# Optimization experiments

Hardware: AMD Instinct MI355X
Metric: run time of the kernel (lower is better)

## Reference

```python
import jax, jax.numpy as jnp
import numpy as np

N_HEADS = 8
D_MODEL = 128
EPS = 1e-6


def setup_inputs() -> dict:
    key = jax.random.key(0)
    k1, k2, k3, k4, k5 = jax.random.split(key, 5)
    B, Dim, F, T = 1, D_MODEL, 256, 1024
    queries = jax.random.normal(k1, (B, Dim, F, T), dtype=jnp.float32)
    keys = jax.random.normal(k2, (B, Dim, F, T), dtype=jnp.float32)
    values = jax.random.normal(k3, (B, Dim, F, T), dtype=jnp.float32)
    # out_projection: Linear(d_model, d_output) with d_output == d_model
    W_out = jax.random.normal(k4, (D_MODEL, D_MODEL), dtype=jnp.float32) / np.sqrt(D_MODEL)
    b_out = jax.random.normal(k5, (D_MODEL,), dtype=jnp.float32) * 0.01
    return {"queries": queries, "keys": keys, "values": values,
            "W_out": W_out, "b_out": b_out}


def _to_heads(x, B, Dim, L, H):
    # (B, Dim, F, T) -> (B, L, Dim) -> (B, L, H, d) -> (B, H, L, d)
    return x.reshape(B, Dim, L).transpose(0, 2, 1).reshape(B, L, H, Dim // H).transpose(0, 2, 1, 3)


def reference(queries, keys, values, W_out, b_out):
    B, Dim, F, T = queries.shape
    L = F * T
    H = N_HEADS
    q = jax.nn.sigmoid(_to_heads(queries, B, Dim, L, H))  # (B,H,L,d)
    k = jax.nn.sigmoid(_to_heads(keys, B, Dim, L, H))
    v = _to_heads(values, B, Dim, L, H)

    # NOTE: sums are over the HEAD axis (dim=1), faithful to the original code
    ks = k.sum(axis=1, keepdims=True)                      # (B,1,L,d)
    qs = q.sum(axis=1, keepdims=True)
    sink_incoming = 1.0 / jnp.sum((q + EPS) * (ks + EPS), axis=-1)      # (B,H,L)
    source_outgoing = 1.0 / jnp.sum((k + EPS) * (qs + EPS), axis=-1)    # (B,H,L)
    conserved_sink = jnp.sum(
        (q + EPS) * ((k * source_outgoing[..., None]).sum(axis=1, keepdims=True) + EPS),
        axis=-1)                                                        # (B,H,L)
    conserved_source = jnp.sum(
        (k + EPS) * ((q * sink_incoming[..., None]).sum(axis=1, keepdims=True) + EPS),
        axis=-1)
    conserved_source = jnp.clip(conserved_source, -1.0, 1.0)
    sink_allocation = jax.nn.sigmoid(conserved_sink * (float(L) / float(L)))
    source_competition = jax.nn.softmax(conserved_source, axis=-1) * float(L)

    kv = jnp.einsum('bhld,bhlm->bhdm', k, v * source_competition[..., None])
    qkv = jnp.einsum('bhld,bhdm->bhlm', q * sink_incoming[..., None], kv)
    x = (qkv * sink_allocation[..., None]).transpose(0, 2, 1, 3).reshape(B, L, Dim)
    x = x @ W_out.T + b_out                                 # dropout is identity (eval)
    return x.transpose(0, 2, 1).reshape(B, Dim, F, T)
```

## Files before the change

kernel.cpp:

```cpp
#include <hip/hip_runtime.h>
#include <hip/hip_bf16.h>

#define L_TOT (1 << 18)
#define L_SHIFT 18
#define NHEAD 8
#define DHEAD 16
#define DMODEL 128
#define EPSF 1e-6f

typedef float f32x4 __attribute__((ext_vector_type(4)));
typedef short bf16x8 __attribute__((ext_vector_type(8)));

__device__ __forceinline__ float frcp(float x) { return __builtin_amdgcn_rcpf(x); }
__device__ __forceinline__ float sigm(float x) { return frcp(1.0f + __expf(-x)); }
__device__ __forceinline__ unsigned short f2bf(float f) {
    return (unsigned short)((__float_as_uint(f) + 0x8000u) >> 16);
}

__device__ __forceinline__ float wsum16(float x) {
    x += __int_as_float(__builtin_amdgcn_update_dpp(0, __float_as_int(x), 0xB1, 0xf, 0xf, true));
    x += __int_as_float(__builtin_amdgcn_update_dpp(0, __float_as_int(x), 0x4E, 0xf, 0xf, true));
    x += __int_as_float(__builtin_amdgcn_update_dpp(0, __float_as_int(x), 0x141, 0xf, 0xf, true));
    x += __int_as_float(__builtin_amdgcn_update_dpp(0, __float_as_int(x), 0x140, 0xf, 0xf, true));
    return x;
}
__device__ __forceinline__ float xadd16(float x) {
    return x + __int_as_float(__builtin_amdgcn_ds_swizzle(__float_as_int(x), 0x401f));
}
__device__ __forceinline__ float xadd32(float x, int bpa) {
    return x + __int_as_float(__builtin_amdgcn_ds_bpermute(bpa, __float_as_int(x)));
}

__global__ __launch_bounds__(256) void k1_stats(
        const float* __restrict__ Q, const float* __restrict__ K,
        float* __restrict__ scale_o, float* __restrict__ wbuf,
        float* __restrict__ sep) {
    __shared__ unsigned int sp[64][128];
    __shared__ float wlds[8][64];
    __shared__ float slds[8][64];
    __shared__ float hred[32];

    const int t = threadIdx.x;
    const int l0 = blockIdx.x * 64;
    const int c = t & 63;
    const int w = t >> 6;
    const int sw = (c & 31) << 2;

#pragma unroll
    for (int i = 0; i < 8; ++i) {
        const int pb = 4 * (w + 4 * i);
        unsigned int pk[4];
#pragma unroll
        for (int r = 0; r < 4; ++r) {
            float qv = sigm(Q[((pb + r) << L_SHIFT) + l0 + c]);
            float kv = sigm(K[((pb + r) << L_SHIFT) + l0 + c]);
            unsigned qu = __float_as_uint(qv) + 0x8000u;
            unsigned ku = __float_as_uint(kv) + 0x8000u;
            pk[r] = (ku & 0xffff0000u) | (qu >> 16);
        }
        *(uint4*)(&sp[c][pb ^ sw]) = make_uint4(pk[0], pk[1], pk[2], pk[3]);
    }
    __syncthreads();

    const int lane = t & 63;
    const int bpa = (lane ^ 32) << 2;
    float acc0 = 0.f, acc1 = 0.f;

    for (int j = 0; j < 16; ++j) {
        const int cl = w * 16 + j;
        const int swl = (cl & 31) << 2;
        const unsigned u0 = sp[cl][lane ^ swl];
        const unsigned u1 = sp[cl][(lane + 64) ^ swl];
        const float sq0 = __uint_as_float(u0 << 16);
        const float sk0 = __uint_as_float(u0 & 0xffff0000u);
        const float sq1 = __uint_as_float(u1 << 16);
        const float sk1 = __uint_as_float(u1 & 0xffff0000u);

        float tks = xadd32(xadd16(sk0 + sk1), bpa);
        float tqs = xadd32(xadd16(sq0 + sq1), bpa);

        const float si0 = frcp(wsum16((sq0 + EPSF) * (tks + EPSF)));
        const float si1 = frcp(wsum16((sq1 + EPSF) * (tks + EPSF)));
        const float so0 = frcp(wsum16((sk0 + EPSF) * (tqs + EPSF)));
        const float so1 = frcp(wsum16((sk1 + EPSF) * (tqs + EPSF)));

        const float tkso = xadd32(xadd16(sk0 * so0 + sk1 * so1), bpa);
        const float tqsi = xadd32(xadd16(sq0 * si0 + sq1 * si1), bpa);

        const float ck0 = wsum16((sq0 + EPSF) * (tkso + EPSF));
        const float ck1 = wsum16((sq1 + EPSF) * (tkso + EPSF));
        float cs0 = wsum16((sk0 + EPSF) * (tqsi + EPSF));
        float cs1 = wsum16((sk1 + EPSF) * (tqsi + EPSF));
        cs0 = fminf(fmaxf(cs0, -1.f), 1.f);
        cs1 = fminf(fmaxf(cs1, -1.f), 1.f);
        const float e0 = __expf(cs0);
        const float e1 = __expf(cs1);
        acc0 += e0; acc1 += e1;
        const float sc0 = sigm(ck0) * si0;
        const float sc1 = sigm(ck1) * si1;

        if ((lane & 15) == 0) {
            const int h = lane >> 4;
            wlds[h][cl] = e0;  wlds[h + 4][cl] = e1;
            slds[h][cl] = sc0; slds[h + 4][cl] = sc1;
        }
    }
    if ((lane & 15) == 0) {
        const int h = lane >> 4;
        hred[w * 8 + h] = acc0;
        hred[w * 8 + h + 4] = acc1;
    }
    __syncthreads();

#pragma unroll
    for (int i = 0; i < 2; ++i) {
        const int idx = t + i * 256;
        const int h = idx >> 6, cc = idx & 63;
        wbuf[(h << L_SHIFT) + l0 + cc] = wlds[h][cc];
        scale_o[(h << L_SHIFT) + l0 + cc] = slds[h][cc];
    }
    if (t < 8)
        sep[blockIdx.x * 8 + t] = hred[t] + hred[8 + t] + hred[16 + t] + hred[24 + t];
}

__global__ __launch_bounds__(256) void k2_kv(
        const float* __restrict__ Kg, const float* __restrict__ Vg,
        const float* __restrict__ wg, float* __restrict__ kv) {
    const int b = blockIdx.x;
    const int h = b >> 7;
    const int blk = b & 127;
    const int t = threadIdx.x;
    const int dd = t >> 4, m = t & 15;

    __shared__ float A[16][132];
    __shared__ float Vv[16][132];
    __shared__ float wl[128];

    const int baseK = (h * DHEAD) << L_SHIFT;
    float acc = 0.f;

    for (int ch = 0; ch < 16; ++ch) {
        const int l0 = blk * 2048 + ch * 128;
        __syncthreads();
        if (t < 128) wl[t] = wg[(h << L_SHIFT) + l0 + t];
        __syncthreads();
#pragma unroll
        for (int i = 0; i < 8; ++i) {
            const int e = t + i * 256;
            const int r = e >> 7, cc = e & 127;
            A[r][cc] = sigm(Kg[baseK + (r << L_SHIFT) + l0 + cc]) * wl[cc];
            Vv[r][cc] = Vg[baseK + (r << L_SHIFT) + l0 + cc];
        }
        __syncthreads();
#pragma unroll
        for (int c4 = 0; c4 < 32; ++c4) {
            const float4 av = *(const float4*)&A[dd][c4 * 4];
            const float4 vv = *(const float4*)&Vv[m][c4 * 4];
            acc += av.x * vv.x + av.y * vv.y + av.z * vv.z + av.w * vv.w;
        }
    }
    atomicAdd(&kv[h * 256 + dd * 16 + m], acc);
}

__global__ __launch_bounds__(256) void k3_wkv(
        const float* __restrict__ Wg, const float* __restrict__ kv,
        const float* __restrict__ sep, unsigned* __restrict__ wkvb) {
    const int hb = blockIdx.x;
    const int t = threadIdx.x;
    __shared__ float kvf[256];
    __shared__ float redl[4];

    float p = 0.f;
#pragma unroll
    for (int i = 0; i < 16; ++i) p += sep[(t + i * 256) * 8 + hb];
#pragma unroll
    for (int o = 32; o >= 1; o >>= 1) p += __shfl_xor(p, o, 64);
    if ((t & 63) == 0) redl[t >> 6] = p;
    __syncthreads();
    const float s = (float)L_TOT / (redl[0] + redl[1] + redl[2] + redl[3]);

    kvf[t] = kv[hb * 256 + t] * s;
    __syncthreads();
#pragma unroll
    for (int i = 0; i < 4; ++i) {
        const int j = t + i * 256;
        const int dim = j & 127, prp = j >> 7;
        float a0 = 0.f, a1 = 0.f;
#pragma unroll
        for (int mm = 0; mm < 16; ++mm) {
            const float wv = Wg[dim * 128 + hb * 16 + mm];
            a0 += wv * kvf[(2 * prp) * 16 + mm];
            a1 += wv * kvf[(2 * prp + 1) * 16 + mm];
        }
        wkvb[dim * 64 + hb * 8 + prp] = ((unsigned)f2bf(a1) << 16) | f2bf(a0);
    }
}

__global__ __launch_bounds__(256) void k4_mfma(
        const float* __restrict__ Q, const float* __restrict__ scale_g,
        const unsigned* __restrict__ wkvb, const float* __restrict__ bg,
        float* __restrict__ out) {
    __shared__ unsigned A_lds[128 * 68];
    __shared__ float bias[128];
    const int t = threadIdx.x;

#pragma unroll
    for (int i = 0; i < 8; ++i) {
        const int idx4 = t + i * 256;
        const uint4 v = ((const uint4*)wkvb)[idx4];
        const int row = idx4 >> 4, c4 = idx4 & 15;
        *(uint4*)&A_lds[row * 68 + c4 * 4] = v;
    }
    if (t < 128) bias[t] = bg[t];
    __syncthreads();

    const int w = t >> 6, lane = t & 63;
    const int lq = lane & 15, lh = lane >> 4;

#pragma unroll
    for (int ci = 0; ci < 2; ++ci) {
        const int l = blockIdx.x * 128 + ci * 64 + w * 16 + lq;

        float qv[4][8];
        float scv[4];
#pragma unroll
        for (int ks = 0; ks < 4; ++ks) {
            scv[ks] = scale_g[((ks * 2 + (lane >> 5)) << L_SHIFT) + l];
#pragma unroll
            for (int j = 0; j < 8; ++j) {
                const int p = ks * 32 + lh * 8 + j;
                qv[ks][j] = Q[(p << L_SHIFT) + l];
            }
        }
        bf16x8 bfr[4];
#pragma unroll
        for (int ks = 0; ks < 4; ++ks)
#pragma unroll
            for (int j = 0; j < 8; ++j)
                bfr[ks][j] = (short)f2bf(sigm(qv[ks][j]) * scv[ks]);

        f32x4 acc[8];
#pragma unroll
        for (int mt = 0; mt < 8; ++mt)
            acc[mt] = *(const f32x4*)&bias[mt * 16 + lh * 4];

#pragma unroll
        for (int ks = 0; ks < 4; ++ks) {
#pragma unroll
            for (int mt = 0; mt < 8; ++mt) {
                const int row = mt * 16 + lq;
                const bf16x8 a = *(const bf16x8*)&A_lds[row * 68 + ks * 16 + lh * 4];
                acc[mt] = __builtin_amdgcn_mfma_f32_16x16x32_bf16(a, bfr[ks], acc[mt], 0, 0, 0);
            }
        }

#pragma unroll
        for (int mt = 0; mt < 8; ++mt) {
#pragma unroll
            for (int r = 0; r < 4; ++r) {
                const int dim = mt * 16 + lh * 4 + r;
                out[(dim << L_SHIFT) + l] = acc[mt][r];
            }
        }
    }
}

extern "C" void kernel_launch(void* const* d_in, const int* in_sizes, int n_in,
                              void* d_out, int out_size, void* d_ws, size_t ws_size,
                              hipStream_t stream) {
    const float* Q = (const float*)d_in[0];
    const float* K = (const float*)d_in[1];
    const float* V = (const float*)d_in[2];
    const float* W = (const float*)d_in[3];
    const float* B = (const float*)d_in[4];
    float* out = (float*)d_out;
    float* ws = (float*)d_ws;

    float* kv       = ws;
    unsigned* wkvb  = (unsigned*)(ws + 2048);
    float* sep      = ws + 10240;
    float* scale    = ws + 43008;
    float* wbuf     = scale + 8 * L_TOT;

    hipMemsetAsync(kv, 0, 2048 * sizeof(float), stream);

    k1_stats<<<L_TOT / 64, 256, 0, stream>>>(Q, K, scale, wbuf, sep);
    k2_kv<<<NHEAD * 128, 256, 0, stream>>>(K, V, wbuf, kv);
    k3_wkv<<<NHEAD, 256, 0, stream>>>(W, kv, sep, wkvb);
    k4_mfma<<<L_TOT / 128, 256, 0, stream>>>(Q, scale, wkvb, B, out);
}
```

Before: 217.2 us.

## Restructure stats kernel thread mapping and replace kv atomics with partial-sum buffer

The stats kernel now assigns four threads per position, each holding 4 of the 16 head dims across all heads in registers. This swaps most cross-lane swizzle/bpermute reductions for in-register sums plus a short 4-lane DPP reduce, and the per-head exp sums are reduced from LDS with shuffles. The kv kernel uses float4 global loads, launches half as many blocks each covering twice the sequence, and writes per-block partials that the wkv kernel sums, removing the memset and atomics. Register pressure in k1 rises, and k3 takes on a serial 64-element reduction per thread.

```diff
diff --git a/kernel.cpp b/kernel.cpp
--- a/kernel.cpp
+++ b/kernel.cpp
@@ -17,18 +17,10 @@
     return (unsigned short)((__float_as_uint(f) + 0x8000u) >> 16);
 }
 
-__device__ __forceinline__ float wsum16(float x) {
+__device__ __forceinline__ float qsum(float x) {
     x += __int_as_float(__builtin_amdgcn_update_dpp(0, __float_as_int(x), 0xB1, 0xf, 0xf, true));
     x += __int_as_float(__builtin_amdgcn_update_dpp(0, __float_as_int(x), 0x4E, 0xf, 0xf, true));
-    x += __int_as_float(__builtin_amdgcn_update_dpp(0, __float_as_int(x), 0x141, 0xf, 0xf, true));
-    x += __int_as_float(__builtin_amdgcn_update_dpp(0, __float_as_int(x), 0x140, 0xf, 0xf, true));
     return x;
-}
-__device__ __forceinline__ float xadd16(float x) {
-    return x + __int_as_float(__builtin_amdgcn_ds_swizzle(__float_as_int(x), 0x401f));
-}
-__device__ __forceinline__ float xadd32(float x, int bpa) {
-    return x + __int_as_float(__builtin_amdgcn_ds_bpermute(bpa, __float_as_int(x)));
 }
 
 __global__ __launch_bounds__(256) void k1_stats(
@@ -38,79 +30,116 @@
     __shared__ unsigned int sp[64][128];
     __shared__ float wlds[8][64];
     __shared__ float slds[8][64];
-    __shared__ float hred[32];
 
     const int t = threadIdx.x;
     const int l0 = blockIdx.x * 64;
-    const int c = t & 63;
-    const int w = t >> 6;
+
+    {
+        const int cS = t & 63;
+        const int w = t >> 6;
+        const int swS = (cS & 31) << 2;
+#pragma unroll
+        for (int i = 0; i < 8; ++i) {
+            const int pb = 4 * (w + 4 * i);
+            unsigned pk[4];
+#pragma unroll
+            for (int r = 0; r < 4; ++r) {
+                float qv = sigm(Q[((pb + r) << L_SHIFT) + l0 + cS]);
+                float kv = sigm(K[((pb + r) << L_SHIFT) + l0 + cS]);
+                unsigned qu = __float_as_uint(qv) + 0x8000u;
+                unsigned ku = __float_as_uint(kv) + 0x8000u;
+                pk[r] = (ku & 0xffff0000u) | (qu >> 16);
+            }
+            *(uint4*)(&sp[cS][pb ^ swS]) = make_uint4(pk[0], pk[1], pk[2], pk[3]);
+        }
+    }
+    __syncthreads();
+
+    const int c = t >> 2;
+    const int s = t & 3;
     const int sw = (c & 31) << 2;
 
-#pragma unroll
-    for (int i = 0; i < 8; ++i) {
-        const int pb = 4 * (w + 4 * i);
-        unsigned int pk[4];
-#pragma unroll
-        for (int r = 0; r < 4; ++r) {
-            float qv = sigm(Q[((pb + r) << L_SHIFT) + l0 + c]);
-            float kv = sigm(K[((pb + r) << L_SHIFT) + l0 + c]);
-            unsigned qu = __float_as_uint(qv) + 0x8000u;
-            unsigned ku = __float_as_uint(kv) + 0x8000u;
-            pk[r] = (ku & 0xffff0000u) | (qu >> 16);
-        }
-        *(uint4*)(&sp[c][pb ^ sw]) = make_uint4(pk[0], pk[1], pk[2], pk[3]);
-    }
-    __syncthreads();
-
-    const int lane = t & 63;
-    const int bpa = (lane ^ 32) << 2;
-    float acc0 = 0.f, acc1 = 0.f;
-
-    for (int j = 0; j < 16; ++j) {
-        const int cl = w * 16 + j;
-        const int swl = (cl & 31) << 2;
-        const unsigned u0 = sp[cl][lane ^ swl];
-        const unsigned u1 = sp[cl][(lane + 64) ^ swl];
-        const float sq0 = __uint_as_float(u0 << 16);
-        const float sk0 = __uint_as_float(u0 & 0xffff0000u);
-        const float sq1 = __uint_as_float(u1 << 16);
-        const float sk1 = __uint_as_float(u1 & 0xffff0000u);
-
-        float tks = xadd32(xadd16(sk0 + sk1), bpa);
-        float tqs = xadd32(xadd16(sq0 + sq1), bpa);
-
-        const float si0 = frcp(wsum16((sq0 + EPSF) * (tks + EPSF)));
-        const float si1 = frcp(wsum16((sq1 + EPSF) * (tks + EPSF)));
-        const float so0 = frcp(wsum16((sk0 + EPSF) * (tqs + EPSF)));
-        const float so1 = frcp(wsum16((sk1 + EPSF) * (tqs + EPSF)));
-
-        const float tkso = xadd32(xadd16(sk0 * so0 + sk1 * so1), bpa);
-        const float tqsi = xadd32(xadd16(sq0 * si0 + sq1 * si1), bpa);
-
-        const float ck0 = wsum16((sq0 + EPSF) * (tkso + EPSF));
-        const float ck1 = wsum16((sq1 + EPSF) * (tkso + EPSF));
-        float cs0 = wsum16((sk0 + EPSF) * (tqsi + EPSF));
-        float cs1 = wsum16((sk1 + EPSF) * (tqsi + EPSF));
-        cs0 = fminf(fmaxf(cs0, -1.f), 1.f);
-        cs1 = fminf(fmaxf(cs1, -1.f), 1.f);
-        const float e0 = __expf(cs0);
-        const float e1 = __expf(cs1);
-        acc0 += e0; acc1 += e1;
-        const float sc0 = sigm(ck0) * si0;
-        const float sc1 = sigm(ck1) * si1;
-
-        if ((lane & 15) == 0) {
-            const int h = lane >> 4;
-            wlds[h][cl] = e0;  wlds[h + 4][cl] = e1;
-            slds[h][cl] = sc0; slds[h + 4][cl] = sc1;
-        }
-    }
-    if ((lane & 15) == 0) {
-        const int h = lane >> 4;
-        hred[w * 8 + h] = acc0;
-        hred[w * 8 + h + 4] = acc1;
-    }
-    __syncthreads();
+    unsigned a[32];
+#pragma unroll
+    for (int h = 0; h < 8; ++h) {
+        const uint4 v = *(const uint4*)&sp[c][(h * 16 + s * 4) ^ sw];
+        a[h * 4 + 0] = v.x; a[h * 4 + 1] = v.y;
+        a[h * 4 + 2] = v.z; a[h * 4 + 3] = v.w;
+    }
+
+    float ks[4] = {0.f, 0.f, 0.f, 0.f}, qs[4] = {0.f, 0.f, 0.f, 0.f};
+#pragma unroll
+    for (int h = 0; h < 8; ++h)
+#pragma unroll
+        for (int j = 0; j < 4; ++j) {
+            const unsigned u = a[h * 4 + j];
+            qs[j] += __uint_as_float(u << 16);
+            ks[j] += __uint_as_float(u & 0xffff0000u);
+        }
+
+    float kse[4], qse[4];
+#pragma unroll
+    for (int j = 0; j < 4; ++j) { kse[j] = ks[j] + EPSF; qse[j] = qs[j] + EPSF; }
+
+    float si[8], so[8];
+#pragma unroll
+    for (int h = 0; h < 8; ++h) {
+        float aq = 0.f, ak = 0.f;
+#pragma unroll
+        for (int j = 0; j < 4; ++j) {
+            const unsigned u = a[h * 4 + j];
+            aq += (__uint_as_float(u << 16) + EPSF) * kse[j];
+            ak += (__uint_as_float(u & 0xffff0000u) + EPSF) * qse[j];
+        }
+        si[h] = frcp(qsum(aq));
+        so[h] = frcp(qsum(ak));
+    }
+
+    float kso[4] = {0.f, 0.f, 0.f, 0.f}, qsi[4] = {0.f, 0.f, 0.f, 0.f};
+#pragma unroll
+    for (int h = 0; h < 8; ++h)
+#pragma unroll
+        for (int j = 0; j < 4; ++j) {
+            const unsigned u = a[h * 4 + j];
+            kso[j] += __uint_as_float(u & 0xffff0000u) * so[h];
+            qsi[j] += __uint_as_float(u << 16) * si[h];
+        }
+#pragma unroll
+    for (int j = 0; j < 4; ++j) { kse[j] = kso[j] + EPSF; qse[j] = qsi[j] + EPSF; }
+
+    float e2[2], sc2[2];
+#pragma unroll
+    for (int h = 0; h < 8; ++h) {
+        float aq = 0.f, ak = 0.f;
+#pragma unroll
+        for (int j = 0; j < 4; ++j) {
+            const unsigned u = a[h * 4 + j];
+            aq += (__uint_as_float(u << 16) + EPSF) * kse[j];
+            ak += (__uint_as_float(u & 0xffff0000u) + EPSF) * qse[j];
+        }
+        const float ck = qsum(aq);
+        float cs = qsum(ak);
+        if ((h >> 1) == s) {
+            cs = fminf(fmaxf(cs, -1.f), 1.f);
+            e2[h & 1] = __expf(cs);
+            sc2[h & 1] = sigm(ck) * si[h];
+        }
+    }
+    wlds[2 * s + 0][c] = e2[0];
+    wlds[2 * s + 1][c] = e2[1];
+    slds[2 * s + 0][c] = sc2[0];
+    slds[2 * s + 1][c] = sc2[1];
+    __syncthreads();
+
+    {
+        float v = wlds[t >> 5][t & 31] + wlds[t >> 5][32 + (t & 31)];
+        v += __shfl_xor(v, 16, 64);
+        v += __shfl_xor(v, 8, 64);
+        v += __shfl_xor(v, 4, 64);
+        v += __shfl_xor(v, 2, 64);
+        v += __shfl_xor(v, 1, 64);
+        if ((t & 31) == 0) sep[blockIdx.x * 8 + (t >> 5)] = v;
+    }
 
 #pragma unroll
     for (int i = 0; i < 2; ++i) {
@@ -119,16 +148,14 @@
         wbuf[(h << L_SHIFT) + l0 + cc] = wlds[h][cc];
         scale_o[(h << L_SHIFT) + l0 + cc] = slds[h][cc];
     }
-    if (t < 8)
-        sep[blockIdx.x * 8 + t] = hred[t] + hred[8 + t] + hred[16 + t] + hred[24 + t];
 }
 
 __global__ __launch_bounds__(256) void k2_kv(
         const float* __restrict__ Kg, const float* __restrict__ Vg,
-        const float* __restrict__ wg, float* __restrict__ kv) {
+        const float* __restrict__ wg, float* __restrict__ parts) {
     const int b = blockIdx.x;
-    const int h = b >> 7;
-    const int blk = b & 127;
+    const int h = b >> 6;
+    const int blk = b & 63;
     const int t = threadIdx.x;
     const int dd = t >> 4, m = t & 15;
 
@@ -139,17 +166,22 @@
     const int baseK = (h * DHEAD) << L_SHIFT;
     float acc = 0.f;
 
-    for (int ch = 0; ch < 16; ++ch) {
-        const int l0 = blk * 2048 + ch * 128;
+    for (int ch = 0; ch < 32; ++ch) {
+        const int l0 = blk * 4096 + ch * 128;
         __syncthreads();
         if (t < 128) wl[t] = wg[(h << L_SHIFT) + l0 + t];
         __syncthreads();
 #pragma unroll
-        for (int i = 0; i < 8; ++i) {
+        for (int i = 0; i < 2; ++i) {
             const int e = t + i * 256;
-            const int r = e >> 7, cc = e & 127;
-            A[r][cc] = sigm(Kg[baseK + (r << L_SHIFT) + l0 + cc]) * wl[cc];
-            Vv[r][cc] = Vg[baseK + (r << L_SHIFT) + l0 + cc];
+            const int r = e >> 5, c4 = e & 31;
+            const float4 kq = *(const float4*)&Kg[baseK + (r << L_SHIFT) + l0 + c4 * 4];
+            const float4 vq = *(const float4*)&Vg[baseK + (r << L_SHIFT) + l0 + c4 * 4];
+            A[r][c4 * 4 + 0] = sigm(kq.x) * wl[c4 * 4 + 0];
+            A[r][c4 * 4 + 1] = sigm(kq.y) * wl[c4 * 4 + 1];
+            A[r][c4 * 4 + 2] = sigm(kq.z) * wl[c4 * 4 + 2];
+            A[r][c4 * 4 + 3] = sigm(kq.w) * wl[c4 * 4 + 3];
+            *(float4*)&Vv[r][c4 * 4] = vq;
         }
         __syncthreads();
 #pragma unroll
@@ -159,11 +191,11 @@
             acc += av.x * vv.x + av.y * vv.y + av.z * vv.z + av.w * vv.w;
         }
     }
-    atomicAdd(&kv[h * 256 + dd * 16 + m], acc);
+    parts[b * 256 + t] = acc;
 }
 
 __global__ __launch_bounds__(256) void k3_wkv(
-        const float* __restrict__ Wg, const float* __restrict__ kv,
+        const float* __restrict__ Wg, const float* __restrict__ parts,
         const float* __restrict__ sep, unsigned* __restrict__ wkvb) {
     const int hb = blockIdx.x;
     const int t = threadIdx.x;
@@ -176,11 +208,16 @@
 #pragma unroll
     for (int o = 32; o >= 1; o >>= 1) p += __shfl_xor(p, o, 64);
     if ((t & 63) == 0) redl[t >> 6] = p;
+
+    float kacc = 0.f;
+    for (int j = 0; j < 64; ++j)
+        kacc += parts[(hb * 64 + j) * 256 + t];
+
     __syncthreads();
     const float s = (float)L_TOT / (redl[0] + redl[1] + redl[2] + redl[3]);
-
-    kvf[t] = kv[hb * 256 + t] * s;
-    __syncthreads();
+    kvf[t] = kacc * s;
+    __syncthreads();
+
 #pragma unroll
     for (int i = 0; i < 4; ++i) {
         const int j = t + i * 256;
@@ -249,8 +286,8 @@
 #pragma unroll
             for (int mt = 0; mt < 8; ++mt) {
                 const int row = mt * 16 + lq;
-                const bf16x8 a = *(const bf16x8*)&A_lds[row * 68 + ks * 16 + lh * 4];
-                acc[mt] = __builtin_amdgcn_mfma_f32_16x16x32_bf16(a, bfr[ks], acc[mt], 0, 0, 0);
+                const bf16x8 aA = *(const bf16x8*)&A_lds[row * 68 + ks * 16 + lh * 4];
+                acc[mt] = __builtin_amdgcn_mfma_f32_16x16x32_bf16(aA, bfr[ks], acc[mt], 0, 0, 0);
             }
         }
 
@@ -276,16 +313,14 @@
     float* out = (float*)d_out;
     float* ws = (float*)d_ws;
 
-    float* kv       = ws;
-    unsigned* wkvb  = (unsigned*)(ws + 2048);
-    float* sep      = ws + 10240;
-    float* scale    = ws + 43008;
+    float* parts    = ws;
+    unsigned* wkvb  = (unsigned*)(ws + 131072);
+    float* sep      = ws + 139264;
+    float* scale    = ws + 172032;
     float* wbuf     = scale + 8 * L_TOT;
 
-    hipMemsetAsync(kv, 0, 2048 * sizeof(float), stream);
-
     k1_stats<<<L_TOT / 64, 256, 0, stream>>>(Q, K, scale, wbuf, sep);
-    k2_kv<<<NHEAD * 128, 256, 0, stream>>>(K, V, wbuf, kv);
-    k3_wkv<<<NHEAD, 256, 0, stream>>>(W, kv, sep, wkvb);
+    k2_kv<<<NHEAD * 64, 256, 0, stream>>>(K, V, wbuf, parts);
+    k3_wkv<<<NHEAD, 256, 0, stream>>>(W, parts, sep, wkvb);
     k4_mfma<<<L_TOT / 128, 256, 0, stream>>>(Q, scale, wkvb, B, out);
 }
```

Measured after the change: 220.1 us. About the same (+1.3%).
